# Kernel tuning notes

Measured on AMD Instinct MI355X. Metric: run time of the kernel, lower is better.

Reference implementation:

```python
import jax, jax.numpy as jnp
import numpy as np

LOC_SIZE, LOC_EMB = 100000, 256
TIM_SIZE, TIM_EMB = 48, 64
UID_SIZE, UID_EMB = 5000, 128
HID = 512
B, T = 64, 128
L_HIST, G = 1024, 4  # 256 history groups of size 4


def setup_inputs() -> dict:
    key = jax.random.key(0)
    ks = jax.random.split(key, 16)
    s = 0.02
    inp = {
        "loc": jax.random.randint(ks[0], (B, T), 0, LOC_SIZE),
        "tim": jax.random.randint(ks[1], (B, T), 0, TIM_SIZE),
        "input_lengths": jax.random.randint(ks[2], (B,), 1, T + 1),
        "history_loc": jax.random.randint(ks[3], (B, L_HIST), 0, LOC_SIZE),
        "history_tim": jax.random.randint(ks[4], (B, L_HIST), 0, TIM_SIZE),
        "history_uid": jax.random.randint(ks[5], (B, L_HIST), 0, UID_SIZE),
        "group_size": G,
        "emb_loc": jax.random.normal(ks[6], (LOC_SIZE, LOC_EMB), jnp.float32) * s,
        "emb_tim": jax.random.normal(ks[7], (TIM_SIZE, TIM_EMB), jnp.float32) * s,
        "emb_uid": jax.random.normal(ks[8], (UID_SIZE, UID_EMB), jnp.float32) * s,
        "W_attn": jax.random.normal(ks[9], (HID, LOC_EMB + TIM_EMB + UID_EMB), jnp.float32) * s,
        "b_attn": jnp.zeros((HID,), jnp.float32),
        "W_ih": jax.random.normal(ks[10], (3 * HID, LOC_EMB + TIM_EMB), jnp.float32) * s,
        "b_ih": jnp.zeros((3 * HID,), jnp.float32),
        "W_hh": jax.random.normal(ks[11], (3 * HID, HID), jnp.float32) * s,
        "b_hh": jnp.zeros((3 * HID,), jnp.float32),
        "W_final": jax.random.normal(ks[12], (UID_SIZE, 3 * HID), jnp.float32) * s,
        "b_final": jnp.zeros((UID_SIZE,), jnp.float32),
    }
    return inp


def _gru(x_seq, W_ih, b_ih, W_hh, b_hh):
    # x_seq: [T, B, Din] -> outputs [T, B, H], PyTorch gate order (r, z, n)
    H = W_hh.shape[1]
    gx = jnp.einsum("tbd,gd->tbg", x_seq, W_ih) + b_ih  # [T,B,3H]
    h0 = jnp.zeros((x_seq.shape[1], H), x_seq.dtype)

    def step(h, gx_t):
        gh = h @ W_hh.T + b_hh
        xr, xz, xn = jnp.split(gx_t, 3, axis=-1)
        hr, hz, hn = jnp.split(gh, 3, axis=-1)
        r = jax.nn.sigmoid(xr + hr)
        z = jax.nn.sigmoid(xz + hz)
        n = jnp.tanh(xn + r * hn)
        h_new = (1.0 - z) * n + z * h
        return h_new, h_new

    _, outs = jax.lax.scan(step, h0, gx)
    return outs  # [T,B,H]


def reference(loc, tim, input_lengths, history_loc, history_tim, history_uid,
              group_size, emb_loc, emb_tim, emb_uid, W_attn, b_attn,
              W_ih, b_ih, W_hh, b_hh, W_final, b_final):
    Bn, Tn = loc.shape
    # current-trajectory embeddings -> GRU (dropout is identity in eval)
    x = jnp.concatenate([emb_loc[loc], emb_tim[tim]], axis=-1)  # [B,T,Din]
    outs = _gru(jnp.swapaxes(x, 0, 1), W_ih, b_ih, W_hh, b_hh)  # [T,B,H]
    outs = jnp.swapaxes(outs, 0, 1)                              # [B,T,H]
    last = outs[jnp.arange(Bn), input_lengths - 1]               # [B,H]

    # history pooling: groups of size G; uid emb averaged within group,
    # loc/tim embeddings taken at each group's first element
    Gc = group_size
    n_groups = history_uid.shape[1] // Gc
    uid_h = emb_uid[history_uid].reshape(Bn, n_groups, Gc, -1).mean(axis=2)  # [B,N,Du]
    loc_h = emb_loc[history_loc[:, ::Gc]]                                    # [B,N,Dl]
    tim_h = emb_tim[history_tim[:, ::Gc]]                                    # [B,N,Dt]
    hist = jnp.concatenate([loc_h, tim_h, uid_h], axis=-1)
    hist = jnp.tanh(jnp.einsum("bnd,hd->bnh", hist, W_attn) + b_attn)        # [B,N,H]

    # 'dot' attention: replaces the nested python-loop scoring
    energies = jnp.einsum("bh,bnh->bn", last, hist)
    attn_w = jax.nn.softmax(energies, axis=-1)
    context = jnp.einsum("bn,bnh->bh", attn_w, hist)

    out = jnp.concatenate([last, context, last], axis=-1)  # [B,3H]
    y = out @ W_final.T + b_final                          # [B,U]
    # original assigns y (one row) into score[t] of shape [T,U] -> broadcast over T
    score = jnp.broadcast_to(y[:, None, :], (Bn, Tn, y.shape[-1]))
    return score
```

## Files before the change

kernel.cpp:

```cpp
#include <hip/hip_runtime.h>
#include <hip/hip_bf16.h>


typedef __attribute__((ext_vector_type(8))) short bf16x8;
typedef __attribute__((ext_vector_type(4))) float f32x4;
typedef __attribute__((ext_vector_type(4))) unsigned short u16x4;
typedef __attribute__((ext_vector_type(2))) unsigned long long u64x2;
typedef unsigned long long u64;

__device__ inline unsigned short f2bf(float x) {
  __hip_bfloat16 b = __float2bfloat16(x);
  return __builtin_bit_cast(unsigned short, b);
}
__device__ inline bf16x8 pack8(float4 a, float4 b) {
  bf16x8 w;
  w[0]=(short)f2bf(a.x); w[1]=(short)f2bf(a.y); w[2]=(short)f2bf(a.z); w[3]=(short)f2bf(a.w);
  w[4]=(short)f2bf(b.x); w[5]=(short)f2bf(b.y); w[6]=(short)f2bf(b.z); w[7]=(short)f2bf(b.w);
  return w;
}

__global__ __launch_bounds__(256)
void gemm_gx_f(const int* __restrict__ loc, const int* __restrict__ tim,
               const float* __restrict__ eloc, const float* __restrict__ etim,
               const float* __restrict__ W_ih, const float* __restrict__ b_ih,
               float* __restrict__ gx) {
  constexpr int LDR = 40, K = 320, N = 1536;
  __shared__ short Asl[128 * LDR];
  __shared__ short Bsl[128 * LDR];
  const int tid = threadIdx.x;
  const int lane = tid & 63, wid = tid >> 6;
  const int wr = wid >> 1, wc = wid & 1;
  const int m16 = lane & 15, g4 = lane >> 4;
  const int bm = blockIdx.y * 128, bn = blockIdx.x * 128;
  const int srow = tid >> 1, shalf = tid & 1;
  const int grow = bm + srow;
  const int t_ = grow >> 6, b_ = grow & 63;
  const float* aloc = eloc + (size_t)loc[b_ * 128 + t_] * 256 + (shalf << 4);
  const float* atim = etim + (size_t)tim[b_ * 128 + t_] * 64 + (shalf << 4);
  const float* bbase = W_ih + (size_t)(bn + srow) * K + (shalf << 4);
  float4 a0, a1, a2, a3, w0, w1, w2, w3;
  {
    a0 = ((const float4*)aloc)[0]; a1 = ((const float4*)aloc)[1];
    a2 = ((const float4*)aloc)[2]; a3 = ((const float4*)aloc)[3];
    w0 = ((const float4*)bbase)[0]; w1 = ((const float4*)bbase)[1];
    w2 = ((const float4*)bbase)[2]; w3 = ((const float4*)bbase)[3];
  }
  f32x4 acc[4][4] = {};
  for (int k0 = 0; k0 < K; k0 += 32) {
    short* arow = Asl + srow * LDR + (shalf << 4);
    *(bf16x8*)(arow)     = pack8(a0, a1);
    *(bf16x8*)(arow + 8) = pack8(a2, a3);
    short* brow = Bsl + srow * LDR + (shalf << 4);
    *(bf16x8*)(brow)     = pack8(w0, w1);
    *(bf16x8*)(brow + 8) = pack8(w2, w3);
    __syncthreads();
    if (k0 + 32 < K) {
      const int kn = k0 + 32;
      const float* ap = (kn < 256) ? (aloc + kn) : (atim + (kn - 256));
      a0 = ((const float4*)ap)[0]; a1 = ((const float4*)ap)[1];
      a2 = ((const float4*)ap)[2]; a3 = ((const float4*)ap)[3];
      const float* bp = bbase + kn;
      w0 = ((const float4*)bp)[0]; w1 = ((const float4*)bp)[1];
      w2 = ((const float4*)bp)[2]; w3 = ((const float4*)bp)[3];
    }
    bf16x8 af[4], bfr[4];
#pragma unroll
    for (int i = 0; i < 4; ++i) {
      af[i]  = *(const bf16x8*)(Asl + ((wr << 6) + (i << 4) + m16) * LDR + (g4 << 3));
      bfr[i] = *(const bf16x8*)(Bsl + ((wc << 6) + (i << 4) + m16) * LDR + (g4 << 3));
    }
#pragma unroll
    for (int i = 0; i < 4; ++i)
#pragma unroll
      for (int j = 0; j < 4; ++j)
        acc[i][j] = __builtin_amdgcn_mfma_f32_16x16x32_bf16(af[i], bfr[j], acc[i][j], 0, 0, 0);
    __syncthreads();
  }
#pragma unroll
  for (int i = 0; i < 4; ++i)
#pragma unroll
    for (int j = 0; j < 4; ++j) {
      const int col = bn + (wc << 6) + (j << 4) + m16;
      const float bv = b_ih[col];
#pragma unroll
      for (int q = 0; q < 4; ++q) {
        const int row = bm + (wr << 6) + (i << 4) + (g4 << 2) + q;
        gx[(size_t)row * N + col] = acc[i][j][q] + bv;
      }
    }
}

__global__ __launch_bounds__(256)
void gru_attn(const float* __restrict__ gx, const float* __restrict__ W_hh,
              const float* __restrict__ b_hh, const int* __restrict__ lens,
              short* __restrict__ h_bf, float* __restrict__ lastb,
              unsigned int* __restrict__ flags,
              const int* __restrict__ hloc, const int* __restrict__ htim,
              const int* __restrict__ huid,
              const float* __restrict__ eloc, const float* __restrict__ etim,
              const float* __restrict__ euid,
              const float* __restrict__ W_attn, const float* __restrict__ b_attn,
              const float* __restrict__ Wf, float* __restrict__ Wfold,
              float* __restrict__ histt, float* __restrict__ ctx) {
  __shared__ short smem[6 * 16 * 512];
  const int bid = blockIdx.x;
  const int tid = threadIdx.x;

  if (bid < 64) {
    if (tid >= 128) {
      for (int t = 0; t < 128; ++t) __syncthreads();
      return;
    }
    const int lane = tid & 63, tt = tid >> 6;
    const int c = bid >> 2, grp = bid & 3;
    const int j0 = (c << 5) + (tt << 4);
    const int b0 = grp << 4;
    const int m16 = lane & 15, g4 = lane >> 4;

    for (int gi = 0; gi < 3; ++gi) {
      const float* wg = W_hh + (size_t)(gi * 512 + j0) * 512;
      short* slab = smem + (((gi << 1) + tt) << 13);
      for (int r = 0; r < 16; ++r) {
        int k = lane << 3;
        const float4* src = (const float4*)(wg + (size_t)r * 512 + k);
        int off = ((r << 9) + k) ^ ((r & 7) << 3);
        *(bf16x8*)(slab + off) = pack8(src[0], src[1]);
      }
    }
    __syncthreads();

    const int bcol = b0 + m16;
    const int jr = j0 + (g4 << 2);
    const f32x4 bhr = *(const f32x4*)&b_hh[jr];
    const f32x4 bhz = *(const f32x4*)&b_hh[512 + jr];
    const f32x4 bhn = *(const f32x4*)&b_hh[1024 + jr];
    const int lenb = lens[bcol];
    f32x4 hprev = {0.f, 0.f, 0.f, 0.f};

    unsigned int* gflags = flags + (grp << 8);
    unsigned int* ownflag = gflags + (c << 4);

    for (int t = 0; t < 128; ++t) {
      const float* gxb = gx + ((size_t)t * 64 + bcol) * 1536;
      f32x4 gr = *(const f32x4*)(gxb + jr);
      f32x4 gz = *(const f32x4*)(gxb + 512 + jr);
      f32x4 gn = *(const f32x4*)(gxb + 1024 + jr);
      f32x4 ar = {0.f, 0.f, 0.f, 0.f}, az = ar, an = ar;
      if (t) {
        unsigned tgt = (unsigned)t;
        while (true) {
          unsigned f = tgt;
          if (lane < 16)
            f = __hip_atomic_load(gflags + (lane << 4), __ATOMIC_RELAXED, __HIP_MEMORY_SCOPE_AGENT);
          if (__all((int)(f >= tgt))) break;
        }
        asm volatile("" ::: "memory");

        const u64* hp = (const u64*)(h_bf + ((t & 1) << 15) + (size_t)bcol * 512 + (g4 << 3));
        u64 hu[32];
#pragma unroll
        for (int ks = 0; ks < 16; ++ks) {
          hu[2 * ks]     = __hip_atomic_load(hp + ks * 8,     __ATOMIC_RELAXED, __HIP_MEMORY_SCOPE_AGENT);
          hu[2 * ks + 1] = __hip_atomic_load(hp + ks * 8 + 1, __ATOMIC_RELAXED, __HIP_MEMORY_SCOPE_AGENT);
        }
#define GRU_MFMA(ks)                                                                 \
        {                                                                            \
          u64x2 p; p[0] = hu[2 * (ks)]; p[1] = hu[2 * (ks) + 1];                     \
          bf16x8 hf = __builtin_bit_cast(bf16x8, p);                                 \
          int off = ((m16 << 9) + ((ks) << 5) + (g4 << 3)) ^ ((m16 & 7) << 3);       \
          ar = __builtin_amdgcn_mfma_f32_16x16x32_bf16(*(const bf16x8*)(smem + ((0 + tt) << 13) + off), hf, ar, 0, 0, 0); \
          az = __builtin_amdgcn_mfma_f32_16x16x32_bf16(*(const bf16x8*)(smem + ((2 + tt) << 13) + off), hf, az, 0, 0, 0); \
          an = __builtin_amdgcn_mfma_f32_16x16x32_bf16(*(const bf16x8*)(smem + ((4 + tt) << 13) + off), hf, an, 0, 0, 0); \
        }
        GRU_MFMA(0)  GRU_MFMA(1)  GRU_MFMA(2)  GRU_MFMA(3)
        GRU_MFMA(4)  GRU_MFMA(5)  GRU_MFMA(6)  GRU_MFMA(7)
        GRU_MFMA(8)  GRU_MFMA(9)  GRU_MFMA(10) GRU_MFMA(11)
        GRU_MFMA(12) GRU_MFMA(13) GRU_MFMA(14) GRU_MFMA(15)
#undef GRU_MFMA
      }
      u16x4 hw;
#pragma unroll
      for (int q = 0; q < 4; ++q) {
        float r = 1.f / (1.f + __expf(-(gr[q] + ar[q] + bhr[q])));
        float z = 1.f / (1.f + __expf(-(gz[q] + az[q] + bhz[q])));
        float xn = gn[q] + r * (an[q] + bhn[q]);
        float n = 1.f - 2.f / (__expf(2.f * xn) + 1.f);
        float hv = (1.f - z) * n + z * hprev[q];
        hprev[q] = hv;
        hw[q] = f2bf(hv);
      }
      __hip_atomic_store((u64*)(h_bf + ((~t & 1) << 15) + (size_t)bcol * 512 + jr),
                         __builtin_bit_cast(u64, hw),
                         __ATOMIC_RELAXED, __HIP_MEMORY_SCOPE_AGENT);
      if (t == lenb - 1) {
        *(f32x4*)(lastb + (size_t)bcol * 512 + jr) = hprev;
      }
      if (t < 127) {
        asm volatile("s_waitcnt vmcnt(0)" ::: "memory");
        __syncthreads();
        if (tid == 0)
          __hip_atomic_store(ownflag, (unsigned)(t + 1), __ATOMIC_RELAXED, __HIP_MEMORY_SCOPE_AGENT);
      }
    }
    asm volatile("s_waitcnt vmcnt(0)" ::: "memory");
    if (lane == 0)
      __hip_atomic_fetch_add(flags + 2064, 1u, __ATOMIC_RELEASE, __HIP_MEMORY_SCOPE_AGENT);
    return;
  }

  {
    constexpr int LDR = 40, K = 448, N = 512;
    short* Asl = smem;
    short* Bsl = smem + 128 * LDR;
    const int lane = tid & 63, wid = tid >> 6;
    const int wr = wid >> 1, wc = wid & 1;
    const int m16 = lane & 15, g4 = lane >> 4;
    const int srow = tid >> 1, shalf = tid & 1;
    for (int tile = bid - 64; tile < 512; tile += 128) {
      const int yt = tile >> 2, nt = tile & 3;
      const int bm = yt << 7, bn = nt << 7;
      f32x4 acc[4][4] = {};
      for (int k0 = 0; k0 < K; k0 += 32) {
        {
          const int grow = bm + srow;
          const int b = grow >> 8, n = grow & 255;
          const int base = b * 1024 + (n << 2);
          float4 f0, f1, f2, f3;
          if (k0 < 256) {
            const float* ap = eloc + (size_t)hloc[base] * 256 + k0 + (shalf << 4);
            f0 = ((const float4*)ap)[0]; f1 = ((const float4*)ap)[1];
            f2 = ((const float4*)ap)[2]; f3 = ((const float4*)ap)[3];
          } else if (k0 < 320) {
            const float* ap = etim + (size_t)htim[base] * 64 + (k0 - 256) + (shalf << 4);
            f0 = ((const float4*)ap)[0]; f1 = ((const float4*)ap)[1];
            f2 = ((const float4*)ap)[2]; f3 = ((const float4*)ap)[3];
          } else {
            const int cu = (k0 - 320) + (shalf << 4);
            const float4* u0 = (const float4*)(euid + (size_t)huid[base + 0] * 128 + cu);
            const float4* u1 = (const float4*)(euid + (size_t)huid[base + 1] * 128 + cu);
            const float4* u2 = (const float4*)(euid + (size_t)huid[base + 2] * 128 + cu);
            const float4* u3 = (const float4*)(euid + (size_t)huid[base + 3] * 128 + cu);
#define AVG4(idx, dst) { float4 a=u0[idx],b4=u1[idx],c4=u2[idx],d4=u3[idx];            \
            dst.x=0.25f*(a.x+b4.x+c4.x+d4.x); dst.y=0.25f*(a.y+b4.y+c4.y+d4.y);       \
            dst.z=0.25f*(a.z+b4.z+c4.z+d4.z); dst.w=0.25f*(a.w+b4.w+c4.w+d4.w); }
            AVG4(0, f0) AVG4(1, f1) AVG4(2, f2) AVG4(3, f3)
#undef AVG4
          }
          short* arow = Asl + srow * LDR + (shalf << 4);
          *(bf16x8*)(arow)     = pack8(f0, f1);
          *(bf16x8*)(arow + 8) = pack8(f2, f3);
          const float* bp = W_attn + (size_t)(bn + srow) * K + k0 + (shalf << 4);
          f0 = ((const float4*)bp)[0]; f1 = ((const float4*)bp)[1];
          f2 = ((const float4*)bp)[2]; f3 = ((const float4*)bp)[3];
          short* brow = Bsl + srow * LDR + (shalf << 4);
          *(bf16x8*)(brow)     = pack8(f0, f1);
          *(bf16x8*)(brow + 8) = pack8(f2, f3);
        }
        __syncthreads();
        bf16x8 af[4], bfr[4];
#pragma unroll
        for (int i = 0; i < 4; ++i) {
          af[i]  = *(const bf16x8*)(Asl + ((wr << 6) + (i << 4) + m16) * LDR + (g4 << 3));
          bfr[i] = *(const bf16x8*)(Bsl + ((wc << 6) + (i << 4) + m16) * LDR + (g4 << 3));
        }
#pragma unroll
        for (int i = 0; i < 4; ++i)
#pragma unroll
          for (int j = 0; j < 4; ++j)
            acc[i][j] = __builtin_amdgcn_mfma_f32_16x16x32_bf16(af[i], bfr[j], acc[i][j], 0, 0, 0);
        __syncthreads();
      }
#pragma unroll
      for (int i = 0; i < 4; ++i)
#pragma unroll
        for (int j = 0; j < 4; ++j) {
          const int col = bn + (wc << 6) + (j << 4) + m16;
          const float bv = b_attn[col];
#pragma unroll
          for (int q = 0; q < 4; ++q) {
            const int row = bm + (wr << 6) + (i << 4) + (g4 << 2) + q;
            histt[(size_t)row * N + col] = tanhf(acc[i][j][q] + bv);
          }
        }
    }
    asm volatile("s_waitcnt vmcnt(0)" ::: "memory");
    if (tid == 0)
      __hip_atomic_fetch_add(flags + 2048, 1u, __ATOMIC_RELEASE, __HIP_MEMORY_SCOPE_AGENT);

    for (int u = bid - 64; u < 5000; u += 128) {
      const int cc = tid << 1;
      float2 a = *(const float2*)(Wf + (size_t)u * 1536 + cc);
      float2 b2 = *(const float2*)(Wf + (size_t)u * 1536 + 1024 + cc);
      float2 o; o.x = a.x + b2.x; o.y = a.y + b2.y;
      *(float2*)(Wfold + (size_t)u * 512 + cc) = o;
    }
  }

  if (bid < 128) {
    if (tid == 0) {
      while (true) {
        unsigned a = __hip_atomic_load(flags + 2048, __ATOMIC_RELAXED, __HIP_MEMORY_SCOPE_AGENT);
        unsigned g = __hip_atomic_load(flags + 2064, __ATOMIC_RELAXED, __HIP_MEMORY_SCOPE_AGENT);
        if (a >= 128u && g >= 128u) break;
        __builtin_amdgcn_s_sleep(7);
      }
    }
    __syncthreads();
    __builtin_amdgcn_fence(__ATOMIC_ACQUIRE, "agent");
    const int b = bid - 64;
    float* ls  = (float*)smem;
    float* wv  = ls + 512;
    float* red = wv + 256;
    ((float2*)ls)[tid] = ((const float2*)(lastb + (size_t)b * 512))[tid];
    __syncthreads();
    const float* hb = histt + (size_t)b * 256 * 512;
    const float* hrow = hb + (size_t)tid * 512;
    float acc = 0.f;
    for (int k = 0; k < 512; k += 4) {
      float4 h4 = *(const float4*)(hrow + k);
      acc += ls[k] * h4.x + ls[k + 1] * h4.y + ls[k + 2] * h4.z + ls[k + 3] * h4.w;
    }
    red[tid] = acc;
    __syncthreads();
    for (int s = 128; s; s >>= 1) {
      if (tid < s) red[tid] = fmaxf(red[tid], red[tid + s]);
      __syncthreads();
    }
    float m = red[0];
    __syncthreads();
    float ex = expf(acc - m);
    wv[tid] = ex; red[tid] = ex;
    __syncthreads();
    for (int s = 128; s; s >>= 1) {
      if (tid < s) red[tid] += red[tid + s];
      __syncthreads();
    }
    float inv = 1.f / red[0];
    float c0 = 0.f, c1 = 0.f;
    for (int n = 0; n < 256; ++n) {
      float wn = wv[n];
      c0 += wn * hb[(size_t)n * 512 + tid];
      c1 += wn * hb[(size_t)n * 512 + tid + 256];
    }
    ctx[(size_t)b * 512 + tid]       = c0 * inv;
    ctx[(size_t)b * 512 + tid + 256] = c1 * inv;
  }
}

__global__ __launch_bounds__(256)
void final_gemm(const float* __restrict__ last, const float* __restrict__ ctx,
                const float* __restrict__ Wfold, const float* __restrict__ Wf,
                const float* __restrict__ bf, float* __restrict__ y) {
  __shared__ float s[64][132];
  const int tid = threadIdx.x;
  const int u0 = blockIdx.x << 3;
  const int ul = tid >> 6, b = tid & 63;
  float acc0 = 0.f, acc1 = 0.f;
  for (int kc = 0; kc < 8; ++kc) {
    __syncthreads();
    for (int i = tid; i < 2048; i += 256) {
      int rb = i >> 5, cc = (i & 31) << 2;
      int k = kc * 128 + cc;
      const float* src = (k < 512) ? (last + (size_t)rb * 512 + k)
                                   : (ctx + (size_t)rb * 512 + k - 512);
      *(float4*)&s[rb][cc] = *(const float4*)src;
    }
    __syncthreads();
#pragma unroll
    for (int uu = 0; uu < 2; ++uu) {
      int u = u0 + ul + uu * 4;
      const float* wrow = (kc < 4) ? (Wfold + (size_t)u * 512 + kc * 128)
                                   : (Wf + (size_t)u * 1536 + 512 + (kc - 4) * 128);
      float a = 0.f;
#pragma unroll 8
      for (int c = 0; c < 128; c += 4) {
        float4 w4 = *(const float4*)(wrow + c);
        float4 s4 = *(const float4*)&s[b][c];
        a += w4.x * s4.x + w4.y * s4.y + w4.z * s4.z + w4.w * s4.w;
      }
      if (uu == 0) acc0 += a; else acc1 += a;
    }
  }
  int u = u0 + ul;
  y[(size_t)b * 5000 + u]     = acc0 + bf[u];
  y[(size_t)b * 5000 + u + 4] = acc1 + bf[u + 4];
}

__global__ void broadcast_y(const float* __restrict__ y, float* __restrict__ out) {
  int bt = blockIdx.x;
  const float4* src = (const float4*)(y + (size_t)(bt >> 7) * 5000);
  float4* dst = (float4*)(out + (size_t)bt * 5000);
  for (int i = threadIdx.x; i < 1250; i += 256) dst[i] = src[i];
}

extern "C" void kernel_launch(void* const* d_in, const int* in_sizes, int n_in,
                              void* d_out, int out_size, void* d_ws, size_t ws_size,
                              hipStream_t stream) {
  const int* loc  = (const int*)d_in[0];
  const int* tim  = (const int*)d_in[1];
  const int* lens = (const int*)d_in[2];
  const int* hloc = (const int*)d_in[3];
  const int* htim = (const int*)d_in[4];
  const int* huid = (const int*)d_in[5];
  const float* eloc    = (const float*)d_in[7];
  const float* etim    = (const float*)d_in[8];
  const float* euid    = (const float*)d_in[9];
  const float* W_attn  = (const float*)d_in[10];
  const float* b_attn  = (const float*)d_in[11];
  const float* W_ih    = (const float*)d_in[12];
  const float* b_ih    = (const float*)d_in[13];
  const float* W_hh    = (const float*)d_in[14];
  const float* b_hh    = (const float*)d_in[15];
  const float* W_final = (const float*)d_in[16];
  const float* b_final = (const float*)d_in[17];
  float* out = (float*)d_out;
  char* ws = (char*)d_ws;

  float* gx    = (float*)(ws + 0ull);
  float* histt = (float*)(ws + 50331648ull);
  float* lastb = (float*)(ws + 83886080ull);
  float* ctx   = (float*)(ws + 84017152ull);
  float* yv    = (float*)(ws + 84148224ull);
  short* h_bf  = (short*)(ws + 85428224ull);
  unsigned int* flags = (unsigned int*)(ws + 85559296ull);
  float* Wfold = (float*)(ws + 85571584ull);

  hipMemsetAsync(flags, 0, 12288, stream);
  gemm_gx_f<<<dim3(12, 64), 256, 0, stream>>>(loc, tim, eloc, etim, W_ih, b_ih, gx);

  gru_attn<<<192, 256, 0, stream>>>(gx, W_hh, b_hh, lens, h_bf, lastb, flags,
                                    hloc, htim, huid, eloc, etim, euid,
                                    W_attn, b_attn, W_final, Wfold, histt, ctx);

  final_gemm<<<625, 256, 0, stream>>>(lastb, ctx, Wfold, W_final, b_final, yv);
  broadcast_y<<<8192, 256, 0, stream>>>(yv, out);
}
```

Measured before the change: 616.6 us.

## Stop GRU recurrence at group max length and signal per-batch completion

Each GRU block group now computes the largest input length among its 16 batch rows and runs the recurrent loop only up to that step, instead of always running all 128 steps. The single global GRU-done counter is replaced by per-batch completion counters, bumped when a batch's last step is written. Attention blocks can then start as soon as their own batch row is final rather than waiting for every GRU block. This trims wasted recurrent steps and lets attention overlap the GRU tail, at the cost of a few extra atomics and length scans per step.

```diff
diff --git a/kernel.cpp b/kernel.cpp
--- a/kernel.cpp
+++ b/kernel.cpp
@@ -107,14 +107,19 @@
   const int tid = threadIdx.x;
 
   if (bid < 64) {
+    const int grp0 = bid & 3;
+    const int b00 = grp0 << 4;
+    int tmax = 0;
+    for (int i = 0; i < 16; ++i) tmax = max(tmax, lens[b00 + i]);
+
     if (tid >= 128) {
-      for (int t = 0; t < 128; ++t) __syncthreads();
+      for (int t = 0; t < tmax + 1; ++t) __syncthreads();
       return;
     }
     const int lane = tid & 63, tt = tid >> 6;
-    const int c = bid >> 2, grp = bid & 3;
+    const int c = bid >> 2, grp = grp0;
     const int j0 = (c << 5) + (tt << 4);
-    const int b0 = grp << 4;
+    const int b0 = b00;
     const int m16 = lane & 15, g4 = lane >> 4;
 
     for (int gi = 0; gi < 3; ++gi) {
@@ -139,8 +144,9 @@
 
     unsigned int* gflags = flags + (grp << 8);
     unsigned int* ownflag = gflags + (c << 4);
-
-    for (int t = 0; t < 128; ++t) {
+    unsigned int* bdone = flags + 1024;
+
+    for (int t = 0; t < tmax; ++t) {
       const float* gxb = gx + ((size_t)t * 64 + bcol) * 1536;
       f32x4 gr = *(const f32x4*)(gxb + jr);
       f32x4 gz = *(const f32x4*)(gxb + 512 + jr);
@@ -195,16 +201,26 @@
       if (t == lenb - 1) {
         *(f32x4*)(lastb + (size_t)bcol * 512 + jr) = hprev;
       }
-      if (t < 127) {
+      if (t < tmax - 1) {
         asm volatile("s_waitcnt vmcnt(0)" ::: "memory");
         __syncthreads();
-        if (tid == 0)
+        if (tid == 0) {
           __hip_atomic_store(ownflag, (unsigned)(t + 1), __ATOMIC_RELAXED, __HIP_MEMORY_SCOPE_AGENT);
+          for (int i = 0; i < 16; ++i)
+            if (lens[b0 + i] == t + 1)
+              __hip_atomic_fetch_add(bdone + ((b0 + i) << 4), 1u,
+                                     __ATOMIC_RELAXED, __HIP_MEMORY_SCOPE_AGENT);
+        }
       }
     }
     asm volatile("s_waitcnt vmcnt(0)" ::: "memory");
-    if (lane == 0)
-      __hip_atomic_fetch_add(flags + 2064, 1u, __ATOMIC_RELEASE, __HIP_MEMORY_SCOPE_AGENT);
+    __syncthreads();
+    if (tid == 0) {
+      for (int i = 0; i < 16; ++i)
+        if (lens[b0 + i] == tmax)
+          __hip_atomic_fetch_add(bdone + ((b0 + i) << 4), 1u,
+                                 __ATOMIC_RELAXED, __HIP_MEMORY_SCOPE_AGENT);
+    }
     return;
   }
 
@@ -297,17 +313,15 @@
   }
 
   if (bid < 128) {
+    const int b = bid - 64;
     if (tid == 0) {
-      while (true) {
-        unsigned a = __hip_atomic_load(flags + 2048, __ATOMIC_RELAXED, __HIP_MEMORY_SCOPE_AGENT);
-        unsigned g = __hip_atomic_load(flags + 2064, __ATOMIC_RELAXED, __HIP_MEMORY_SCOPE_AGENT);
-        if (a >= 128u && g >= 128u) break;
+      while (__hip_atomic_load(flags + 2048, __ATOMIC_RELAXED, __HIP_MEMORY_SCOPE_AGENT) < 128u)
         __builtin_amdgcn_s_sleep(7);
-      }
+      while (__hip_atomic_load(flags + 1024 + (b << 4), __ATOMIC_RELAXED, __HIP_MEMORY_SCOPE_AGENT) < 16u)
+        __builtin_amdgcn_s_sleep(7);
     }
     __syncthreads();
     __builtin_amdgcn_fence(__ATOMIC_ACQUIRE, "agent");
-    const int b = bid - 64;
     float* ls  = (float*)smem;
     float* wv  = ls + 512;
     float* red = wv + 256;
```

Result: faster. 594.1 us (-3.7%).
